# Performance work log

Measured on AMD Instinct MI355X. Metric: run time of the kernel, lower is better.

Reference implementation:

```python
import jax, jax.numpy as jnp
import numpy as np

B, C, F, T = 8, 2, 64, 1024
E = C * F            # embed_dim = 128
H = 8                # num_heads
DH = E // H          # head_dim = 16


def setup_inputs() -> dict:
    key = jax.random.key(0)
    ks = jax.random.split(key, 14)
    s = 0.05  # small init scale for numerical stability
    return {
        "x_re": jax.random.normal(ks[0], (B, C, F, T), jnp.float32),
        "x_im": jax.random.normal(ks[1], (B, C, F, T), jnp.float32),
        "win_re": jax.random.normal(ks[2], (3 * E, E), jnp.float32) * s,
        "win_im": jax.random.normal(ks[3], (3 * E, E), jnp.float32) * s,
        "bin_re": jax.random.normal(ks[4], (3 * E,), jnp.float32) * s,
        "bin_im": jax.random.normal(ks[5], (3 * E,), jnp.float32) * s,
        "wout_re": jax.random.normal(ks[6], (E, E), jnp.float32) * s,
        "wout_im": jax.random.normal(ks[7], (E, E), jnp.float32) * s,
        "bout_re": jax.random.normal(ks[8], (E,), jnp.float32) * s,
        "bout_im": jax.random.normal(ks[9], (E,), jnp.float32) * s,
        "wt_re": jax.random.normal(ks[10], (E, E), jnp.float32) * s,
        "wt_im": jax.random.normal(ks[11], (E, E), jnp.float32) * s,
        "bt_re": jax.random.normal(ks[12], (E,), jnp.float32) * s,
        "bt_im": jax.random.normal(ks[13], (E,), jnp.float32) * s,
    }


def _forward(x_re, x_im, win_re, win_im, bin_re, bin_im,
             wout_re, wout_im, bout_re, bout_im,
             wt_re, wt_im, bt_re, bt_im):
    cplx = lambda r, i: (r + 1j * i).astype(jnp.complex64)
    x = cplx(x_re, x_im)                 # [B,C,F,T]
    win, bin_ = cplx(win_re, win_im), cplx(bin_re, bin_im)
    wout, bout = cplx(wout_re, wout_im), cplx(bout_re, bout_im)
    wt, bt = cplx(wt_re, wt_im), cplx(bt_re, bt_im)

    # flatten(1,2).transpose(1,2): [B,C,F,T] -> [B,E,T] -> [B,T,E]
    xs = jnp.transpose(x.reshape(B, E, T), (0, 2, 1))

    # packed complex qkv projection
    qkv = xs @ win.T + bin_              # [B,T,3E]
    q, k, v = jnp.split(qkv, 3, axis=-1)
    split_heads = lambda t: jnp.transpose(t.reshape(B, T, H, DH), (0, 2, 1, 3))
    q, k, v = split_heads(q), split_heads(k), split_heads(v)  # [B,H,T,DH]

    # complex attention scores Q K^H; softmax over real part
    scores = jnp.einsum("bhqd,bhkd->bhqk", q, jnp.conj(k)) * (DH ** -0.5)
    attn = jax.nn.softmax(scores.real, axis=-1).astype(jnp.complex64)
    o = jnp.einsum("bhqk,bhkd->bhqd", attn, v)               # [B,H,T,DH]
    o = jnp.transpose(o, (0, 2, 1, 3)).reshape(B, T, E)
    o = o @ wout.T + bout                # attention out-proj

    # transform: complex Linear E -> E
    y = o @ wt.T + bt                    # [B,T,E]

    # unflatten(-1,(C,F)) then movedim(1,-1): [B,T,C,F] -> [B,C,F,T]
    y = jnp.moveaxis(y.reshape(B, T, C, F), 1, -1)
    return jnp.stack([y.real, y.imag], axis=0)  # [2,B,C,F,T]


def reference(x_re, x_im, win_re, win_im, bin_re, bin_im,
              wout_re, wout_im, bout_re, bout_im,
              wt_re, wt_im, bt_re, bt_im):
    return _forward(x_re, x_im, win_re, win_im, bin_re, bin_im,
                    wout_re, wout_im, bout_re, bout_im,
                    wt_re, wt_im, bt_re, bt_im)
```

## Files before the change

kernel.cpp:

```cpp
#include <hip/hip_runtime.h>
#include <hip/hip_bf16.h>

#define B 8
#define T 1024
#define E 128
#define H 8
#define DH 16
#define E3 384

typedef __attribute__((ext_vector_type(8))) short short8;
typedef __attribute__((ext_vector_type(4))) short short4s;
typedef __attribute__((ext_vector_type(4))) float f32x4;

static __device__ inline short bf16s(float x) {
    union { float f; unsigned u; } v; v.f = x;
    unsigned r = v.u + 0x7fffu + ((v.u >> 16) & 1u);
    return (short)(r >> 16);
}

#if __has_builtin(__builtin_amdgcn_exp2f)
static __device__ inline float fexp2(float x) { return __builtin_amdgcn_exp2f(x); }
#else
static __device__ inline float fexp2(float x) { return __builtin_exp2f(x); }
#endif

static __device__ inline __hip_bfloat162 pk2(float a, float b) {
    float2 t; t.x = a; t.y = b;
    return __float22bfloat162_rn(t);
}

static __device__ inline void stage16(const void* g, void* l) {
    __builtin_amdgcn_global_load_lds(
        (const __attribute__((address_space(1))) void*)g,
        (__attribute__((address_space(3))) void*)l,
        16, 0, 0);
}

#define QSCALE 0.36067376022224085f

__global__ void pack_win_kernel(
    const float* __restrict__ win_re, const float* __restrict__ win_im,
    short* __restrict__ Wp_re, short* __restrict__ Wp_im)
{
    int idx = blockIdx.x * 256 + threadIdx.x;
    int j = idx >> 7, e = idx & 127;
    float wr = win_re[idx], wi = win_im[idx];
    Wp_re[j*256 + e]       = bf16s(wr);
    Wp_re[j*256 + 128 + e] = bf16s(-wi);
    Wp_im[j*256 + e]       = bf16s(wi);
    Wp_im[j*256 + 128 + e] = bf16s(wr);
}

__global__ __launch_bounds__(256) void qkv_fuse_kernel(
    const float* __restrict__ x_re, const float* __restrict__ x_im,
    const short* __restrict__ Wp_re, const short* __restrict__ Wp_im,
    const float* __restrict__ bin_re, const float* __restrict__ bin_im,
    const float* __restrict__ wout_re, const float* __restrict__ wout_im,
    const float* __restrict__ bout_re, const float* __restrict__ bout_im,
    const float* __restrict__ wt_re,   const float* __restrict__ wt_im,
    const float* __restrict__ bt_re,   const float* __restrict__ bt_im,
    short* __restrict__ Qpk, short* __restrict__ Kpk,
    short* __restrict__ Vtre, short* __restrict__ Vtim,
    short* __restrict__ Wfp_re, short* __restrict__ Wfp_im,
    float* __restrict__ bf_re, float* __restrict__ bf_im)
{
    int bid = blockIdx.x;
    int tid = threadIdx.x;

    if (bid < 512) {
        int wave = tid >> 6, lane = tid & 63;
        int col  = lane & 15, quad = lane >> 4;
        int ttile = bid;
        int b  = ttile >> 6;
        int tb = (ttile & 63) * 16 + col;

        short8 xf[8];
        #pragma unroll
        for (int kt = 0; kt < 8; ++kt) {
            const float* xs = (kt < 4) ? x_re : x_im;
            const float* p = &xs[((long)(b*E + (kt & 3)*32 + quad*8))*T + tb];
            float v0 = p[0], v1 = p[(long)T], v2 = p[2L*T], v3 = p[3L*T];
            float v4 = p[4L*T], v5 = p[5L*T], v6 = p[6L*T], v7 = p[7L*T];
            __hip_bfloat162* xp = (__hip_bfloat162*)&xf[kt];
            xp[0] = pk2(v0, v1); xp[1] = pk2(v2, v3);
            xp[2] = pk2(v4, v5); xp[3] = pk2(v6, v7);
        }

        const f32x4 zero = {0.f,0.f,0.f,0.f};

        #pragma unroll
        for (int half = 0; half < 2; ++half) {
            const short* Wsel = half ? Wp_im : Wp_re;
            const float* bias = half ? bin_im : bin_re;

            for (int ni = 0; ni < 6; ++ni) {
                int jt = wave * 6 + ni;
                const short* wrow = &Wsel[(jt*16 + col)*256 + quad*8];
                f32x4 acc = zero;
                #pragma unroll
                for (int kt = 0; kt < 8; ++kt) {
                    short8 af = *(const short8*)(wrow + kt*32);
                    acc = __builtin_amdgcn_mfma_f32_16x16x32_bf16(af, xf[kt], acc, 0, 0, 0);
                }
                int which = jt >> 3;
                int h = jt & 7;
                float scale = (which == 0) ? QSCALE : 1.0f;
                f32x4 res;
                #pragma unroll
                for (int r = 0; r < 4; ++r) {
                    int jg = which*128 + h*16 + quad*4 + r;
                    res[r] = (acc[r] + bias[jg]) * scale;
                }
                long bh = b*H + h;
                if (which == 2) {
                    short* vt = half ? Vtim : Vtre;
                    int tloc = tb & 31, tblk = tb & ~31;
                    int u  = tloc & 15;
                    int kk = (u >> 2)*8 + (u & 3) + ((tloc >= 16) ? 4 : 0);
                    #pragma unroll
                    for (int r = 0; r < 4; ++r)
                        vt[(bh*DH + quad*4 + r)*T + tblk + kk] = bf16s(res[r]);
                } else {
                    short* qk = (which == 0) ? Qpk : Kpk;
                    short4s pk;
                    __hip_bfloat162* pp = (__hip_bfloat162*)&pk;
                    pp[0] = pk2(res[0], res[1]);
                    pp[1] = pk2(res[2], res[3]);
                    *(short4s*)&qk[(bh*T + tb)*32 + half*16 + quad*4] = pk;
                }
            }
        }
    } else if (bid < 576) {
        int idx = (bid - 512) * 256 + tid;
        int j = idx >> 7, e = idx & 127;
        float ar = 0.f, ai = 0.f;
        for (int m = 0; m < E; ++m) {
            float tr = wt_re[j*E+m], ti = wt_im[j*E+m];
            float pr = wout_re[m*E+e], pi = wout_im[m*E+e];
            ar += tr*pr - ti*pi;
            ai += tr*pi + ti*pr;
        }
        Wfp_re[j*256 + e]       = bf16s(ar);
        Wfp_re[j*256 + 128 + e] = bf16s(-ai);
        Wfp_im[j*256 + e]       = bf16s(ai);
        Wfp_im[j*256 + 128 + e] = bf16s(ar);
    } else {
        if (tid < E) {
            float br = bt_re[tid], bi = bt_im[tid];
            for (int m = 0; m < E; ++m) {
                float tr = wt_re[tid*E+m], ti = wt_im[tid*E+m];
                br += tr*bout_re[m] - ti*bout_im[m];
                bi += tr*bout_im[m] + ti*bout_re[m];
            }
            bf_re[tid] = br; bf_im[tid] = bi;
        }
    }
}

__global__ __launch_bounds__(256, 2) void attn_mfma_kernel(
    const short* __restrict__ Qpk, const short* __restrict__ Kpk,
    const short* __restrict__ Vtre, const short* __restrict__ Vtim,
    short* __restrict__ Opk)
{
    __shared__ short lbuf[2][4][512];

    int id   = blockIdx.x;
    int bh   = id & 63;
    int q0   = (id >> 6) * 128;
    int tid  = threadIdx.x;
    int wave = tid >> 6;
    int lane = tid & 63;
    int col  = lane & 15;
    int quad = lane >> 4;

    long kq_base = (long)bh * T * 32;
    int qbase = q0 + wave * 32;

    short8 qfA = *(const short8*)&Qpk[kq_base + (long)(qbase + col)*32 + quad*8];
    short8 qfB = *(const short8*)&Qpk[kq_base + (long)(qbase + 16 + col)*32 + quad*8];

    const short* gsrc;
    int gstep;
    if (wave == 0)      { gsrc = &Kpk[kq_base + col*32 + quad*8];              gstep = 1024; }
    else if (wave == 1) { gsrc = &Kpk[kq_base + 512 + col*32 + quad*8];        gstep = 1024; }
    else if (wave == 2) { gsrc = &Vtre[(long)bh*DH*T + (long)col*T + quad*8];  gstep = 32; }
    else                { gsrc = &Vtim[(long)bh*DH*T + (long)col*T + quad*8];  gstep = 32; }

    short8 ones;
    #pragma unroll
    for (int i = 0; i < 8; ++i) ones[i] = (short)0x3F80;

    f32x4 oAr = {0,0,0,0}, oAi = {0,0,0,0}, lA = {0,0,0,0};
    f32x4 oBr = {0,0,0,0}, oBi = {0,0,0,0}, lB = {0,0,0,0};
    const f32x4 zero = {0.f,0.f,0.f,0.f};

    stage16(gsrc, &lbuf[0][wave][0]);
    gsrc += gstep;
    __syncthreads();

    for (int i = 0; i < 32; ++i) {
        int p = i & 1;
        stage16(gsrc, &lbuf[p^1][wave][0]);
        gsrc += gstep;

        short8 kf0 = *(const short8*)&lbuf[p][0][lane*8];
        short8 kf1 = *(const short8*)&lbuf[p][1][lane*8];
        short8 vr  = *(const short8*)&lbuf[p][2][lane*8];
        short8 vi  = *(const short8*)&lbuf[p][3][lane*8];

        __builtin_amdgcn_s_setprio(1);
        f32x4 sA0 = __builtin_amdgcn_mfma_f32_16x16x32_bf16(kf0, qfA, zero, 0, 0, 0);
        f32x4 sA1 = __builtin_amdgcn_mfma_f32_16x16x32_bf16(kf1, qfA, zero, 0, 0, 0);
        f32x4 sB0 = __builtin_amdgcn_mfma_f32_16x16x32_bf16(kf0, qfB, zero, 0, 0, 0);
        f32x4 sB1 = __builtin_amdgcn_mfma_f32_16x16x32_bf16(kf1, qfB, zero, 0, 0, 0);
        __builtin_amdgcn_s_setprio(0);

        short8 pfA, pfB;
        {
            __hip_bfloat162* pa = (__hip_bfloat162*)&pfA;
            pa[0] = pk2(fexp2(sA0[0]), fexp2(sA0[1]));
            pa[1] = pk2(fexp2(sA0[2]), fexp2(sA0[3]));
            pa[2] = pk2(fexp2(sA1[0]), fexp2(sA1[1]));
            pa[3] = pk2(fexp2(sA1[2]), fexp2(sA1[3]));
            __hip_bfloat162* pb = (__hip_bfloat162*)&pfB;
            pb[0] = pk2(fexp2(sB0[0]), fexp2(sB0[1]));
            pb[1] = pk2(fexp2(sB0[2]), fexp2(sB0[3]));
            pb[2] = pk2(fexp2(sB1[0]), fexp2(sB1[1]));
            pb[3] = pk2(fexp2(sB1[2]), fexp2(sB1[3]));
        }

        __builtin_amdgcn_s_setprio(1);
        oAr = __builtin_amdgcn_mfma_f32_16x16x32_bf16(vr, pfA, oAr, 0, 0, 0);
        oAi = __builtin_amdgcn_mfma_f32_16x16x32_bf16(vi, pfA, oAi, 0, 0, 0);
        lA  = __builtin_amdgcn_mfma_f32_16x16x32_bf16(ones, pfA, lA, 0, 0, 0);
        oBr = __builtin_amdgcn_mfma_f32_16x16x32_bf16(vr, pfB, oBr, 0, 0, 0);
        oBi = __builtin_amdgcn_mfma_f32_16x16x32_bf16(vi, pfB, oBi, 0, 0, 0);
        lB  = __builtin_amdgcn_mfma_f32_16x16x32_bf16(ones, pfB, lB, 0, 0, 0);
        __builtin_amdgcn_s_setprio(0);

        __syncthreads();
    }

    int b = bh >> 3, h = bh & 7;
    float invA = 1.0f / lA[0];
    float invB = 1.0f / lB[0];

    long orowA = ((long)(b*T + qbase + col))*256 + h*16 + quad*4;
    {
        short4s pr, pi_;
        __hip_bfloat162* a = (__hip_bfloat162*)&pr;
        a[0] = pk2(oAr[0]*invA, oAr[1]*invA);
        a[1] = pk2(oAr[2]*invA, oAr[3]*invA);
        __hip_bfloat162* c = (__hip_bfloat162*)&pi_;
        c[0] = pk2(oAi[0]*invA, oAi[1]*invA);
        c[1] = pk2(oAi[2]*invA, oAi[3]*invA);
        *(short4s*)&Opk[orowA]       = pr;
        *(short4s*)&Opk[orowA + 128] = pi_;
    }
    long orowB = orowA + 16L*256;
    {
        short4s pr, pi_;
        __hip_bfloat162* a = (__hip_bfloat162*)&pr;
        a[0] = pk2(oBr[0]*invB, oBr[1]*invB);
        a[1] = pk2(oBr[2]*invB, oBr[3]*invB);
        __hip_bfloat162* c = (__hip_bfloat162*)&pi_;
        c[0] = pk2(oBi[0]*invB, oBi[1]*invB);
        c[1] = pk2(oBi[2]*invB, oBi[3]*invB);
        *(short4s*)&Opk[orowB]       = pr;
        *(short4s*)&Opk[orowB + 128] = pi_;
    }
}

__global__ __launch_bounds__(256) void outproj_mfma_kernel(
    const short* __restrict__ Opk,
    const short* __restrict__ Wfp_re, const short* __restrict__ Wfp_im,
    const float* __restrict__ bf_re, const float* __restrict__ bf_im,
    float* __restrict__ out)
{
    int tid  = threadIdx.x;
    int wave = tid >> 6, lane = tid & 63;
    int col  = lane & 15, quad = lane >> 4;
    int ttile = blockIdx.x;
    int b  = ttile >> 6;
    int tb = (ttile & 63) * 16 + col;
    long trow = (long)b*T + tb;

    short8 xf[8];
    #pragma unroll
    for (int kt = 0; kt < 8; ++kt)
        xf[kt] = *(const short8*)&Opk[trow*256 + kt*32 + quad*8];

    const f32x4 zero = {0.f,0.f,0.f,0.f};
    #pragma unroll
    for (int ni = 0; ni < 4; ++ni) {
        int nt = wave * 4 + ni;
        int is_im = nt >= 8;
        int jt = is_im ? nt - 8 : nt;
        const short* Wsel = is_im ? Wfp_im : Wfp_re;
        const short* wrow = &Wsel[(jt*16 + col)*256 + quad*8];
        f32x4 acc = zero;
        #pragma unroll
        for (int kt = 0; kt < 8; ++kt) {
            short8 af = *(const short8*)(wrow + kt*32);
            acc = __builtin_amdgcn_mfma_f32_16x16x32_bf16(af, xf[kt], acc, 0, 0, 0);
        }
        const float* bias = is_im ? bf_im : bf_re;
        long part = is_im ? (long)B*E*T : 0;
        #pragma unroll
        for (int r = 0; r < 4; ++r) {
            int j = jt*16 + quad*4 + r;
            out[part + ((long)(b*E + j))*T + tb] = acc[r] + bias[j];
        }
    }
}

extern "C" void kernel_launch(void* const* d_in, const int* in_sizes, int n_in,
                              void* d_out, int out_size, void* d_ws, size_t ws_size,
                              hipStream_t stream)
{
    const float* x_re    = (const float*)d_in[0];
    const float* x_im    = (const float*)d_in[1];
    const float* win_re  = (const float*)d_in[2];
    const float* win_im  = (const float*)d_in[3];
    const float* bin_re  = (const float*)d_in[4];
    const float* bin_im  = (const float*)d_in[5];
    const float* wout_re = (const float*)d_in[6];
    const float* wout_im = (const float*)d_in[7];
    const float* bout_re = (const float*)d_in[8];
    const float* bout_im = (const float*)d_in[9];
    const float* wt_re   = (const float*)d_in[10];
    const float* wt_im   = (const float*)d_in[11];
    const float* bt_re   = (const float*)d_in[12];
    const float* bt_im   = (const float*)d_in[13];
    float* out = (float*)d_out;

    short* Qpk  = (short*)d_ws;
    short* Kpk  = Qpk + (long)B*H*T*32;
    short* Vtre = Kpk + (long)B*H*T*32;
    short* Vtim = Vtre + (long)B*H*DH*T;
    short* Opk  = Vtim + (long)B*H*DH*T;
    short* Wp_re  = Opk + (long)B*T*256;
    short* Wp_im  = Wp_re + E3*256;
    short* Wfp_re = Wp_im + E3*256;
    short* Wfp_im = Wfp_re + E*256;
    float* bf_re  = (float*)(Wfp_im + E*256);
    float* bf_im  = bf_re + E;

    pack_win_kernel<<<dim3(E3*E/256), dim3(256), 0, stream>>>(
        win_re, win_im, Wp_re, Wp_im);

    qkv_fuse_kernel<<<dim3(577), dim3(256), 0, stream>>>(
        x_re, x_im, Wp_re, Wp_im, bin_re, bin_im,
        wout_re, wout_im, bout_re, bout_im,
        wt_re, wt_im, bt_re, bt_im,
        Qpk, Kpk, Vtre, Vtim,
        Wfp_re, Wfp_im, bf_re, bf_im);

    attn_mfma_kernel<<<dim3(8 * 64), dim3(256), 0, stream>>>(
        Qpk, Kpk, Vtre, Vtim, Opk);

    outproj_mfma_kernel<<<dim3(512), dim3(256), 0, stream>>>(
        Opk, Wfp_re, Wfp_im, bf_re, bf_im, out);
}
```

Baseline: 142.3 us.

## Retile QKV projection blocks over 64 timesteps and a quarter of output tiles

The QKV projection blocks are remapped. Each block now covers 64 timesteps, staged through shared memory, and a quarter of the output column tiles, instead of 16 timesteps and all columns. Each weight fragment loaded from global memory now feeds four MFMAs (one per timestep subtile), so weight traffic per output drops. Adjacent output tiles also give better write coalescing. In exchange it needs more registers for 32 x-fragments plus 4 accumulators, and launch bounds are set to 2 blocks per SM, which may cause spills.

```diff
diff --git a/kernel.cpp b/kernel.cpp
--- a/kernel.cpp
+++ b/kernel.cpp
@@ -51,7 +51,7 @@
     Wp_im[j*256 + 128 + e] = bf16s(wr);
 }
 
-__global__ __launch_bounds__(256) void qkv_fuse_kernel(
+__global__ __launch_bounds__(256, 2) void qkv_fuse_kernel(
     const float* __restrict__ x_re, const float* __restrict__ x_im,
     const short* __restrict__ Wp_re, const short* __restrict__ Wp_im,
     const float* __restrict__ bin_re, const float* __restrict__ bin_im,
@@ -64,59 +64,82 @@
     short* __restrict__ Wfp_re, short* __restrict__ Wfp_im,
     float* __restrict__ bf_re, float* __restrict__ bf_im)
 {
+    __shared__ short8 xsh[4][8][64];
+
     int bid = blockIdx.x;
     int tid = threadIdx.x;
 
     if (bid < 512) {
         int wave = tid >> 6, lane = tid & 63;
         int col  = lane & 15, quad = lane >> 4;
-        int ttile = bid;
-        int b  = ttile >> 6;
-        int tb = (ttile & 63) * 16 + col;
-
-        short8 xf[8];
+        int jg    = bid & 3;
+        int ttile = bid >> 2;
+        int b  = ttile >> 4;
+        int t0 = (ttile & 15) * 64;
+
+        {
+            int tglob = t0 + wave*16 + col;
+            #pragma unroll
+            for (int kt = 0; kt < 8; ++kt) {
+                const float* xs = (kt < 4) ? x_re : x_im;
+                const float* p = &xs[((long)(b*E + (kt & 3)*32 + quad*8))*T + tglob];
+                float v0 = p[0], v1 = p[(long)T], v2 = p[2L*T], v3 = p[3L*T];
+                float v4 = p[4L*T], v5 = p[5L*T], v6 = p[6L*T], v7 = p[7L*T];
+                short8 xv;
+                __hip_bfloat162* xp = (__hip_bfloat162*)&xv;
+                xp[0] = pk2(v0, v1); xp[1] = pk2(v2, v3);
+                xp[2] = pk2(v4, v5); xp[3] = pk2(v6, v7);
+                xsh[wave][kt][lane] = xv;
+            }
+        }
+        __syncthreads();
+
+        short8 xr[4][8];
         #pragma unroll
-        for (int kt = 0; kt < 8; ++kt) {
-            const float* xs = (kt < 4) ? x_re : x_im;
-            const float* p = &xs[((long)(b*E + (kt & 3)*32 + quad*8))*T + tb];
-            float v0 = p[0], v1 = p[(long)T], v2 = p[2L*T], v3 = p[3L*T];
-            float v4 = p[4L*T], v5 = p[5L*T], v6 = p[6L*T], v7 = p[7L*T];
-            __hip_bfloat162* xp = (__hip_bfloat162*)&xf[kt];
-            xp[0] = pk2(v0, v1); xp[1] = pk2(v2, v3);
-            xp[2] = pk2(v4, v5); xp[3] = pk2(v6, v7);
-        }
+        for (int ts = 0; ts < 4; ++ts)
+            #pragma unroll
+            for (int kt = 0; kt < 8; ++kt)
+                xr[ts][kt] = xsh[ts][kt][lane];
 
         const f32x4 zero = {0.f,0.f,0.f,0.f};
 
-        #pragma unroll
-        for (int half = 0; half < 2; ++half) {
+        for (int ui = 0; ui < 3; ++ui) {
+            int idx  = wave * 3 + ui;
+            int half = idx >= 6;
+            int u    = half ? idx - 6 : idx;
+            int jt   = jg * 6 + u;
             const short* Wsel = half ? Wp_im : Wp_re;
             const float* bias = half ? bin_im : bin_re;
-
-            for (int ni = 0; ni < 6; ++ni) {
-                int jt = wave * 6 + ni;
-                const short* wrow = &Wsel[(jt*16 + col)*256 + quad*8];
-                f32x4 acc = zero;
+            const short* wrow = &Wsel[(jt*16 + col)*256 + quad*8];
+
+            f32x4 acc[4] = {zero, zero, zero, zero};
+            #pragma unroll
+            for (int kt = 0; kt < 8; ++kt) {
+                short8 af = *(const short8*)(wrow + kt*32);
                 #pragma unroll
-                for (int kt = 0; kt < 8; ++kt) {
-                    short8 af = *(const short8*)(wrow + kt*32);
-                    acc = __builtin_amdgcn_mfma_f32_16x16x32_bf16(af, xf[kt], acc, 0, 0, 0);
-                }
-                int which = jt >> 3;
-                int h = jt & 7;
-                float scale = (which == 0) ? QSCALE : 1.0f;
+                for (int ts = 0; ts < 4; ++ts)
+                    acc[ts] = __builtin_amdgcn_mfma_f32_16x16x32_bf16(af, xr[ts][kt], acc[ts], 0, 0, 0);
+            }
+
+            int which = jt >> 3;
+            int h = jt & 7;
+            float scale = (which == 0) ? QSCALE : 1.0f;
+            long bh = b*H + h;
+
+            #pragma unroll
+            for (int ts = 0; ts < 4; ++ts) {
+                int tb = t0 + ts*16 + col;
                 f32x4 res;
                 #pragma unroll
                 for (int r = 0; r < 4; ++r) {
-                    int jg = which*128 + h*16 + quad*4 + r;
-                    res[r] = (acc[r] + bias[jg]) * scale;
+                    int jgl = which*128 + h*16 + quad*4 + r;
+                    res[r] = (acc[ts][r] + bias[jgl]) * scale;
                 }
-                long bh = b*H + h;
                 if (which == 2) {
                     short* vt = half ? Vtim : Vtre;
                     int tloc = tb & 31, tblk = tb & ~31;
-                    int u  = tloc & 15;
-                    int kk = (u >> 2)*8 + (u & 3) + ((tloc >= 16) ? 4 : 0);
+                    int u2 = tloc & 15;
+                    int kk = (u2 >> 2)*8 + (u2 & 3) + ((tloc >= 16) ? 4 : 0);
                     #pragma unroll
                     for (int r = 0; r < 4; ++r)
                         vt[(bh*DH + quad*4 + r)*T + tblk + kk] = bf16s(res[r]);
```

New measurement: 137.7 us. 3.2% less time.
